# Optimization experiments

Measured on AMD Instinct MI355X. Metric: run time of the kernel, lower is better.

Reference implementation:

```python
import jax, jax.numpy as jnp
import numpy as np

SEQ_LEN = 4096
IN_DIM = 1024
QVK_DIM = 1024


def setup_inputs() -> dict:
    key = jax.random.key(0)
    kx, kw = jax.random.split(key)
    x = jax.random.normal(kx, (SEQ_LEN, IN_DIM), dtype=jnp.float32)
    # glorot-uniform-ish scale for W: limit = sqrt(6/(fan_in+fan_out))
    limit = np.sqrt(6.0 / (IN_DIM + 3 * QVK_DIM)).astype(np.float32)
    W = jax.random.uniform(kw, (IN_DIM, 3 * QVK_DIM), dtype=jnp.float32,
                           minval=-limit, maxval=limit)
    return {"x": x, "W": W}


def reference(x, W):
    seq_len = x.shape[0]
    qvk = x @ W                                   # [S, 3*D]
    # NOTE: original splits as queries, VALS, keys (vals is the middle chunk)
    queries, vals, keys = jnp.split(qvk, 3, axis=1)
    raw = (queries @ keys.T) / jnp.sqrt(jnp.float32(QVK_DIM))  # [S, S]
    # causal mask: strictly-upper-triangular entries -> -inf (same as the
    # original's scatter of -inf at triu_indices(seq_len, 1))
    causal = jnp.tril(jnp.ones((seq_len, seq_len), dtype=bool))
    raw = jnp.where(causal, raw, -jnp.inf)
    weights = jax.nn.softmax(raw, axis=1)
    return weights @ vals                         # [S, D]
```

## Files before the change

kernel.cpp:

```cpp
#include <hip/hip_runtime.h>

#define SEQ 4096
#define KDIM 1024
#define NQKV 3072
#define BK 32

typedef __bf16 bf16x8 __attribute__((ext_vector_type(8)));
typedef float  f32x4  __attribute__((ext_vector_type(4)));

#define WAITV(n) asm volatile("s_waitcnt vmcnt(" #n ")" ::: "memory")
#define BAR()    asm volatile("s_barrier" ::: "memory")

__device__ __forceinline__ unsigned short f2b(float f) {
    unsigned int u = __float_as_uint(f);
    u += 0x7FFFu + ((u >> 16) & 1u);
    return (unsigned short)(u >> 16);
}
__device__ __forceinline__ float b2f(unsigned short h) {
    return __uint_as_float(((unsigned int)h) << 16);
}

__device__ __forceinline__ void gld_lds16(const unsigned short* g, unsigned short* l) {
    __builtin_amdgcn_global_load_lds(
        (const __attribute__((address_space(1))) void*)g,
        (__attribute__((address_space(3))) void*)l, 16, 0, 0);
}

__device__ __forceinline__ void stage_tiles(
    const unsigned short* Ag, int lda, const unsigned short* Bg, int ldb,
    int k0, unsigned short* sA, unsigned short* sB, int wave, int lane)
{
    #pragma unroll
    for (int i = 0; i < 2; ++i) {
        int c = i * 512 + wave * 64 + lane;
        int row = c >> 2, slot = c & 3;
        int p = slot ^ ((row >> 1) & 3);
        gld_lds16(Ag + row * lda + k0 + p * 8, sA + (i * 8 + wave) * 512);
        gld_lds16(Bg + row * ldb + k0 + p * 8, sB + (i * 8 + wave) * 512);
    }
}

__device__ __forceinline__ const unsigned short* frag_addr(
    const unsigned short* s, int row, int quad)
{
    return s + row * 32 + (quad ^ ((row >> 1) & 3)) * 8;
}

__device__ __forceinline__ void compute_tile(
    const unsigned short* sA, const unsigned short* sB, f32x4 acc[8][4],
    int wm, int wn, int lr, int quad)
{
    bf16x8 af[8], bq[4];
    #pragma unroll
    for (int j = 0; j < 4; ++j)
        bq[j] = *(const bf16x8*)frag_addr(sB, wn + 16 * j + lr, quad);
    #pragma unroll
    for (int i = 0; i < 8; ++i)
        af[i] = *(const bf16x8*)frag_addr(sA, wm + 16 * i + lr, quad);
    #pragma unroll
    for (int i = 0; i < 8; ++i)
        #pragma unroll
        for (int j = 0; j < 4; ++j)
            acc[i][j] = __builtin_amdgcn_mfma_f32_16x16x32_bf16(af[i], bq[j], acc[i][j], 0, 0, 0);
}

__device__ __forceinline__ void mfma_pipe(
    const unsigned short* Ag, int lda, const unsigned short* Bg, int ldb,
    int kLen, unsigned short* lds, f32x4 acc[8][4])
{
    const int tid  = threadIdx.x;
    const int wave = tid >> 6, lane = tid & 63;
    const int lr   = lane & 15, quad = lane >> 4;
    const int wm   = (wave >> 2) * 128, wn = (wave & 3) * 64;
    const int niter = kLen >> 5;

    #pragma unroll
    for (int s = 0; s < 2; ++s)
        if (s < niter)
            stage_tiles(Ag, lda, Bg, ldb, s * BK,
                        lds + s * 16384, lds + s * 16384 + 8192, wave, lane);

    #pragma unroll 1
    for (int k = 0; k < niter; ++k) {
        if (k + 1 < niter) WAITV(4);
        else               WAITV(0);
        BAR();
        if (k + 2 < niter) {
            const int s = (k + 2) % 3;
            stage_tiles(Ag, lda, Bg, ldb, (k + 2) * BK,
                        lds + s * 16384, lds + s * 16384 + 8192, wave, lane);
        }
        const int c = k % 3;
        compute_tile(lds + c * 16384, lds + c * 16384 + 8192, acc, wm, wn, lr, quad);
    }
}

__device__ __forceinline__ void zero_acc(f32x4 acc[8][4]) {
    const f32x4 z = {0.f, 0.f, 0.f, 0.f};
    #pragma unroll
    for (int i = 0; i < 8; ++i)
        #pragma unroll
        for (int j = 0; j < 4; ++j) acc[i][j] = z;
}

__device__ __forceinline__ void store_rows_bf16(
    f32x4 acc[8][4], unsigned short* Cw, int ld, unsigned short* lw, int lane)
{
    const int lr = lane & 15, quad = lane >> 4;
    #pragma unroll
    for (int i = 0; i < 8; ++i) {
        #pragma unroll
        for (int j = 0; j < 4; ++j)
            #pragma unroll
            for (int r = 0; r < 4; ++r)
                lw[(quad * 4 + r) * 72 + j * 16 + lr] = f2b(acc[i][j][r]);
        #pragma unroll
        for (int t = 0; t < 2; ++t) {
            int chunk = t * 64 + lane;
            int rl = chunk >> 3, c8 = chunk & 7;
            uint4 v = *(const uint4*)(lw + rl * 72 + c8 * 8);
            *(uint4*)(Cw + (16 * i + rl) * ld + c8 * 8) = v;
        }
    }
}

__device__ __forceinline__ void store_cols_bf16(
    f32x4 acc[8][4], unsigned short* Vw, unsigned short* lw, int lane)
{
    const int lr = lane & 15, quad = lane >> 4;
    #pragma unroll
    for (int ip = 0; ip < 4; ++ip) {
        #pragma unroll
        for (int ii = 0; ii < 2; ++ii)
            #pragma unroll
            for (int j = 0; j < 4; ++j)
                #pragma unroll
                for (int r = 0; r < 4; ++r)
                    lw[(j * 16 + lr) * 40 + ii * 16 + quad * 4 + r] = f2b(acc[ip * 2 + ii][j][r]);
        #pragma unroll
        for (int t = 0; t < 4; ++t) {
            int chunk = t * 64 + lane;
            int col = chunk >> 2, c8 = chunk & 3;
            uint4 v = *(const uint4*)(lw + col * 40 + c8 * 8);
            *(uint4*)(Vw + col * SEQ + ip * 32 + c8 * 8) = v;
        }
    }
}

__global__ __launch_bounds__(256) void prep(
    const float* __restrict__ x, unsigned short* __restrict__ Xb,
    const float* __restrict__ W, unsigned short* __restrict__ Wt,
    float4* __restrict__ out, float4* __restrict__ lrow)
{
    __shared__ float tile[32][33];
    const int b = blockIdx.x, tid = threadIdx.x;
    if (b < 4096) {
        int i = (b * 256 + tid) * 4;
        float4 v = *(const float4*)(x + i);
        ushort4 o;
        o.x = f2b(v.x); o.y = f2b(v.y); o.z = f2b(v.z); o.w = f2b(v.w);
        *(ushort4*)(Xb + i) = o;
    } else if (b < 8192) {
        const float4 z = {0.f, 0.f, 0.f, 0.f};
        out[(b - 4096) * 256 + tid] = z;
    } else if (b < 11264) {
        const int bb = b - 8192;
        const int n0 = (bb % 96) * 32, k0 = (bb / 96) * 32;
        const int c = tid & 31, r0 = tid >> 5;
        #pragma unroll
        for (int r = r0; r < 32; r += 8)
            tile[r][c] = W[(k0 + r) * NQKV + n0 + c];
        __syncthreads();
        #pragma unroll
        for (int r = r0; r < 32; r += 8)
            Wt[(n0 + r) * KDIM + k0 + c] = f2b(tile[c][r]);
    } else {
        const float4 z = {0.f, 0.f, 0.f, 0.f};
        #pragma unroll
        for (int k = 0; k < 4; ++k) lrow[tid * 4 + k] = z;
    }
}

__global__ __launch_bounds__(512, 2) void qvk_gemm(
    const unsigned short* __restrict__ Xb, const unsigned short* __restrict__ Wt,
    unsigned short* __restrict__ Qb, unsigned short* __restrict__ Kb,
    unsigned short* __restrict__ Vt)
{
    __shared__ __align__(16) unsigned short lds[49152];
    const int m0 = blockIdx.x * 256;
    const int n0 = blockIdx.y * 256;
    f32x4 acc[8][4];
    zero_acc(acc);
    mfma_pipe(Xb + m0 * KDIM, KDIM, Wt + n0 * KDIM, KDIM, KDIM, lds, acc);
    __syncthreads();

    const int lane = threadIdx.x & 63, wave = threadIdx.x >> 6;
    const int wm = (wave >> 2) * 128, wn = (wave & 3) * 64;
    unsigned short* lw = lds + wave * 2560;
    const int region = n0 >> 10;
    const int nloc = n0 & 1023;
    if (region == 0)
        store_rows_bf16(acc, Qb + (m0 + wm) * KDIM + nloc + wn, KDIM, lw, lane);
    else if (region == 2)
        store_rows_bf16(acc, Kb + (m0 + wm) * KDIM + nloc + wn, KDIM, lw, lane);
    else
        store_cols_bf16(acc, Vt + (nloc + wn) * SEQ + m0 + wm, lw, lane);
}

__global__ __launch_bounds__(512, 2) void score_exp_gemm(
    const unsigned short* __restrict__ Qb, const unsigned short* __restrict__ Kb,
    unsigned short* __restrict__ Sb, float* __restrict__ lrow)
{
    __shared__ __align__(16) unsigned short lds[49152];
    const int bm = blockIdx.x, bn = blockIdx.y;
    if (bn > bm) return;
    const int m0 = bm * 256, n0 = bn * 256;

    f32x4 acc[8][4];
    zero_acc(acc);
    mfma_pipe(Qb + m0 * KDIM, KDIM, Kb + n0 * KDIM, KDIM, KDIM, lds, acc);

    const int lane = threadIdx.x & 63, wave = threadIdx.x >> 6;
    const int lr = lane & 15, quad = lane >> 4;
    const int wm = (wave >> 2) * 128, wn = (wave & 3) * 64;
    #pragma unroll
    for (int i = 0; i < 8; ++i)
        #pragma unroll
        for (int j = 0; j < 4; ++j)
            #pragma unroll
            for (int r = 0; r < 4; ++r) {
                float v = __expf(acc[i][j][r] * 0.03125f);
                if (bm == bn) {
                    int row = wm + 16 * i + quad * 4 + r;
                    int col = wn + 16 * j + lr;
                    if (col > row) v = 0.f;
                }
                acc[i][j][r] = v;
            }
    #pragma unroll
    for (int i = 0; i < 8; ++i)
        #pragma unroll
        for (int r = 0; r < 4; ++r) {
            float s = acc[i][0][r] + acc[i][1][r] + acc[i][2][r] + acc[i][3][r];
            s += __shfl_xor(s, 1, 16);
            s += __shfl_xor(s, 2, 16);
            s += __shfl_xor(s, 4, 16);
            s += __shfl_xor(s, 8, 16);
            if (lr == 0)
                atomicAdd(&lrow[m0 + wm + 16 * i + quad * 4 + r], s);
        }
    __syncthreads();
    store_rows_bf16(acc, Sb + (m0 + wm) * SEQ + n0 + wn, SEQ, lds + wave * 2560, lane);
}

__global__ __launch_bounds__(512, 2) void pv_gemm(
    const unsigned short* __restrict__ Sb, const unsigned short* __restrict__ Vt,
    const float* __restrict__ lrow, float* __restrict__ out)
{
    __shared__ __align__(16) unsigned short lds[49152];
    const int n0 = blockIdx.x * 256;
    const int y = blockIdx.y;
    int mm, c;
    if (y < 4)       { mm = y;                c = 0; }
    else if (y < 12) { mm = 4 + (y - 4) / 2;  c = (y - 4) & 1; }
    else if (y < 24) { mm = 8 + (y - 12) / 3; c = (y - 12) % 3; }
    else             { mm = 12 + (y - 24) / 4; c = (y - 24) & 3; }
    const int m0 = mm * 256;
    const int kstart = c * 1024;
    const int kend = min((mm + 1) * 256, kstart + 1024);
    const int nchunks = (mm >> 2) + 1;

    f32x4 acc[8][4];
    zero_acc(acc);
    mfma_pipe(Sb + m0 * SEQ + kstart, SEQ, Vt + n0 * SEQ + kstart, SEQ,
              kend - kstart, lds, acc);

    const int lane = threadIdx.x & 63, wave = threadIdx.x >> 6;
    const int lr = lane & 15, quad = lane >> 4;
    const int wm = (wave >> 2) * 128, wn = (wave & 3) * 64;
    #pragma unroll
    for (int i = 0; i < 8; ++i) {
        const int rbase = m0 + wm + 16 * i + quad * 4;
        const float4 l4 = *(const float4*)(lrow + rbase);
        float inv[4] = {1.0f / l4.x, 1.0f / l4.y, 1.0f / l4.z, 1.0f / l4.w};
        #pragma unroll
        for (int j = 0; j < 4; ++j) {
            const int col = n0 + wn + 16 * j + lr;
            if (nchunks == 1) {
                #pragma unroll
                for (int r = 0; r < 4; ++r)
                    out[(rbase + r) * KDIM + col] = acc[i][j][r] * inv[r];
            } else {
                #pragma unroll
                for (int r = 0; r < 4; ++r)
                    atomicAdd(&out[(rbase + r) * KDIM + col], acc[i][j][r] * inv[r]);
            }
        }
    }
}

extern "C" void kernel_launch(void* const* d_in, const int* in_sizes, int n_in,
                              void* d_out, int out_size, void* d_ws, size_t ws_size,
                              hipStream_t stream) {
    const float* x = (const float*)d_in[0];
    const float* W = (const float*)d_in[1];
    float* out = (float*)d_out;
    char* ws = (char*)d_ws;

    unsigned short* Xb = (unsigned short*)(ws);
    unsigned short* Wt = (unsigned short*)(ws + 8388608);
    unsigned short* Qb = (unsigned short*)(ws + 14680064);
    unsigned short* Kb = (unsigned short*)(ws + 23068672);
    unsigned short* Vt = (unsigned short*)(ws + 31457280);
    unsigned short* Sb = (unsigned short*)(ws + 39845888);
    float*        lrow = (float*)(ws + 73400320);

    prep          <<<11265, 256, 0, stream>>>(x, Xb, W, Wt, (float4*)out, (float4*)lrow);
    qvk_gemm      <<<dim3(SEQ / 256, NQKV / 256), 512, 0, stream>>>(Xb, Wt, Qb, Kb, Vt);
    score_exp_gemm<<<dim3(SEQ / 256, SEQ / 256), 512, 0, stream>>>(Qb, Kb, Sb, lrow);
    pv_gemm       <<<dim3(KDIM / 256, 40), 512, 0, stream>>>(Sb, Vt, lrow, out);
}
```

Measured before the change: 202.9 us.

## Restructure GEMM mainloop into half-tile ping-pong stages with priority hints

After: 211.7 us. 1.04x slower.

```diff
diff --git a/kernel.cpp b/kernel.cpp
--- a/kernel.cpp
+++ b/kernel.cpp
@@ -3,13 +3,14 @@
 #define SEQ 4096
 #define KDIM 1024
 #define NQKV 3072
-#define BK 32
 
 typedef __bf16 bf16x8 __attribute__((ext_vector_type(8)));
 typedef float  f32x4  __attribute__((ext_vector_type(4)));
 
 #define WAITV(n) asm volatile("s_waitcnt vmcnt(" #n ")" ::: "memory")
+#define LGKM0()  asm volatile("s_waitcnt lgkmcnt(0)" ::: "memory")
 #define BAR()    asm volatile("s_barrier" ::: "memory")
+#define SETP(n)  __builtin_amdgcn_s_setprio(n)
 
 __device__ __forceinline__ unsigned short f2b(float f) {
     unsigned int u = __float_as_uint(f);
@@ -26,18 +27,14 @@
         (__attribute__((address_space(3))) void*)l, 16, 0, 0);
 }
 
-__device__ __forceinline__ void stage_tiles(
-    const unsigned short* Ag, int lda, const unsigned short* Bg, int ldb,
-    int k0, unsigned short* sA, unsigned short* sB, int wave, int lane)
-{
-    #pragma unroll
-    for (int i = 0; i < 2; ++i) {
-        int c = i * 512 + wave * 64 + lane;
-        int row = c >> 2, slot = c & 3;
-        int p = slot ^ ((row >> 1) & 3);
-        gld_lds16(Ag + row * lda + k0 + p * 8, sA + (i * 8 + wave) * 512);
-        gld_lds16(Bg + row * ldb + k0 + p * 8, sB + (i * 8 + wave) * 512);
-    }
+__device__ __forceinline__ void stage_half(
+    const unsigned short* G, int ldg, int h, int k0,
+    unsigned short* slot, int wave, int lane)
+{
+    int c = wave * 64 + lane;
+    int row = c >> 2, sl = c & 3;
+    int p = sl ^ ((row >> 1) & 3);
+    gld_lds16(G + (h * 128 + row) * ldg + k0 + p * 8, slot + wave * 512);
 }
 
 __device__ __forceinline__ const unsigned short* frag_addr(
@@ -46,22 +43,23 @@
     return s + row * 32 + (quad ^ ((row >> 1) & 3)) * 8;
 }
 
-__device__ __forceinline__ void compute_tile(
-    const unsigned short* sA, const unsigned short* sB, f32x4 acc[8][4],
-    int wm, int wn, int lr, int quad)
-{
-    bf16x8 af[8], bq[4];
-    #pragma unroll
-    for (int j = 0; j < 4; ++j)
-        bq[j] = *(const bf16x8*)frag_addr(sB, wn + 16 * j + lr, quad);
-    #pragma unroll
-    for (int i = 0; i < 8; ++i)
-        af[i] = *(const bf16x8*)frag_addr(sA, wm + 16 * i + lr, quad);
-    #pragma unroll
-    for (int i = 0; i < 8; ++i)
+__device__ __forceinline__ void read_frags(
+    bf16x8 v[4], const unsigned short* slot, int r0, int lr, int quad)
+{
+    #pragma unroll
+    for (int i = 0; i < 4; ++i)
+        v[i] = *(const bf16x8*)frag_addr(slot, r0 + 16 * i + lr, quad);
+}
+
+__device__ __forceinline__ void mfma_q(
+    f32x4 acc[8][4], const bf16x8 a[4], const bf16x8 b[4], int ioff)
+{
+    #pragma unroll
+    for (int i = 0; i < 4; ++i)
         #pragma unroll
         for (int j = 0; j < 4; ++j)
-            acc[i][j] = __builtin_amdgcn_mfma_f32_16x16x32_bf16(af[i], bq[j], acc[i][j], 0, 0, 0);
+            acc[ioff + i][j] =
+                __builtin_amdgcn_mfma_f32_16x16x32_bf16(a[i], b[j], acc[ioff + i][j], 0, 0, 0);
 }
 
 __device__ __forceinline__ void mfma_pipe(
@@ -71,27 +69,76 @@
     const int tid  = threadIdx.x;
     const int wave = tid >> 6, lane = tid & 63;
     const int lr   = lane & 15, quad = lane >> 4;
-    const int wm   = (wave >> 2) * 128, wn = (wave & 3) * 64;
-    const int niter = kLen >> 5;
-
-    #pragma unroll
-    for (int s = 0; s < 2; ++s)
-        if (s < niter)
-            stage_tiles(Ag, lda, Bg, ldb, s * BK,
-                        lds + s * 16384, lds + s * 16384 + 8192, wave, lane);
+    const int hA   = wave >> 2;
+    const int hB   = (wave & 3) >> 1;
+    const int bRow = (wave & 1) * 64;
+    unsigned short* lsA = lds;
+    unsigned short* lsB = lds + 16384;
+    const int niter = kLen >> 6;
+
+    stage_half(Bg, ldb, 0, 0,  lsB + 0 * 4096, wave, lane);
+    stage_half(Bg, ldb, 1, 0,  lsB + 1 * 4096, wave, lane);
+    stage_half(Ag, lda, 0, 0,  lsA + 0 * 4096, wave, lane);
+    stage_half(Ag, lda, 1, 0,  lsA + 1 * 4096, wave, lane);
+    stage_half(Bg, ldb, 0, 32, lsB + 2 * 4096, wave, lane);
+    stage_half(Bg, ldb, 1, 32, lsB + 3 * 4096, wave, lane);
+    stage_half(Ag, lda, 0, 32, lsA + 2 * 4096, wave, lane);
+    stage_half(Ag, lda, 1, 32, lsA + 3 * 4096, wave, lane);
+    WAITV(4);
+    BAR();
+
+    const unsigned short* A0 = lsA + hA * 4096;
+    const unsigned short* B0 = lsB + hB * 4096;
+    const unsigned short* A1 = lsA + (2 + hA) * 4096;
+    const unsigned short* B1 = lsB + (2 + hB) * 4096;
+
+    bf16x8 a[4], b[4];
 
     #pragma unroll 1
-    for (int k = 0; k < niter; ++k) {
-        if (k + 1 < niter) WAITV(4);
-        else               WAITV(0);
+    for (int u = 0; u < niter; ++u) {
+        const bool pre = (u + 1 < niter);
+        const int k2 = (2 * u + 2) * 32;
+        const int k3 = (2 * u + 3) * 32;
+
+        read_frags(a, A0, 0, lr, quad);
+        read_frags(b, B0, bRow, lr, quad);
+        LGKM0(); BAR();
+        if (pre) {
+            stage_half(Bg, ldb, 0, k2, lsB + 0 * 4096, wave, lane);
+            stage_half(Bg, ldb, 1, k2, lsB + 1 * 4096, wave, lane);
+        }
+        SETP(1); mfma_q(acc, a, b, 0); SETP(0);
         BAR();
-        if (k + 2 < niter) {
-            const int s = (k + 2) % 3;
-            stage_tiles(Ag, lda, Bg, ldb, (k + 2) * BK,
-                        lds + s * 16384, lds + s * 16384 + 8192, wave, lane);
-        }
-        const int c = k % 3;
-        compute_tile(lds + c * 16384, lds + c * 16384 + 8192, acc, wm, wn, lr, quad);
+
+        read_frags(a, A0, 64, lr, quad);
+        LGKM0(); BAR();
+        if (pre) {
+            stage_half(Ag, lda, 0, k2, lsA + 0 * 4096, wave, lane);
+            stage_half(Ag, lda, 1, k2, lsA + 1 * 4096, wave, lane);
+        }
+        SETP(1); mfma_q(acc, a, b, 4); SETP(0);
+        if (pre) WAITV(4); else WAITV(0);
+        BAR();
+
+        read_frags(a, A1, 0, lr, quad);
+        read_frags(b, B1, bRow, lr, quad);
+        LGKM0(); BAR();
+        if (pre) {
+            stage_half(Bg, ldb, 0, k3, lsB + 2 * 4096, wave, lane);
+            stage_half(Bg, ldb, 1, k3, lsB + 3 * 4096, wave, lane);
+        }
+        SETP(1); mfma_q(acc, a, b, 0); SETP(0);
+        BAR();
+
+        read_frags(a, A1, 64, lr, quad);
+        LGKM0(); BAR();
+        if (pre) {
+            stage_half(Ag, lda, 0, k3, lsA + 2 * 4096, wave, lane);
+            stage_half(Ag, lda, 1, k3, lsA + 3 * 4096, wave, lane);
+        }
+        SETP(1); mfma_q(acc, a, b, 4); SETP(0);
+        if (pre) WAITV(4);
+        BAR();
     }
 }
 
@@ -186,7 +233,7 @@
     unsigned short* __restrict__ Qb, unsigned short* __restrict__ Kb,
     unsigned short* __restrict__ Vt)
 {
-    __shared__ __align__(16) unsigned short lds[49152];
+    __shared__ __align__(16) unsigned short lds[32768];
     const int m0 = blockIdx.x * 256;
     const int n0 = blockIdx.y * 256;
     f32x4 acc[8][4];
@@ -211,7 +258,7 @@
     const unsigned short* __restrict__ Qb, const unsigned short* __restrict__ Kb,
     unsigned short* __restrict__ Sb, float* __restrict__ lrow)
 {
-    __shared__ __align__(16) unsigned short lds[49152];
+    __shared__ __align__(16) unsigned short lds[32768];
     const int bm = blockIdx.x, bn = blockIdx.y;
     if (bn > bm) return;
     const int m0 = bm * 256, n0 = bn * 256;
@@ -257,13 +304,13 @@
     const unsigned short* __restrict__ Sb, const unsigned short* __restrict__ Vt,
     const float* __restrict__ lrow, float* __restrict__ out)
 {
-    __shared__ __align__(16) unsigned short lds[49152];
+    __shared__ __align__(16) unsigned short lds[32768];
     const int n0 = blockIdx.x * 256;
     const int y = blockIdx.y;
     int mm, c;
-    if (y < 4)       { mm = y;                c = 0; }
-    else if (y < 12) { mm = 4 + (y - 4) / 2;  c = (y - 4) & 1; }
-    else if (y < 24) { mm = 8 + (y - 12) / 3; c = (y - 12) % 3; }
+    if (y < 4)       { mm = y;                 c = 0; }
+    else if (y < 12) { mm = 4 + (y - 4) / 2;   c = (y - 4) & 1; }
+    else if (y < 24) { mm = 8 + (y - 12) / 3;  c = (y - 12) % 3; }
     else             { mm = 12 + (y - 24) / 4; c = (y - 24) & 3; }
     const int m0 = mm * 256;
     const int kstart = c * 1024;
```
